# Performance work log

Measured on AMD Instinct MI355X. Metric: run time of the kernel, lower is better.

Reference implementation:

```python
import jax, jax.numpy as jnp
import numpy as np

B, T, N, F = 8, 32, 10000, 16
E = 160000
HG, HT = 64, 128
EPS = 1e-5


def setup_inputs() -> dict:
    key = jax.random.key(0)
    ks = jax.random.split(key, 12)
    s = lambda i, shape, sc=0.05: jax.random.normal(ks[i], shape, dtype=jnp.float32) * sc
    return {
        "x_seq": jax.random.normal(ks[0], (B, T, N, F), dtype=jnp.float32),
        "edge_index": jax.random.randint(ks[1], (2, E), 0, N),
        "W1l": s(2, (HG, F)), "b1": jnp.zeros((HG,), jnp.float32), "W1r": s(3, (HG, F)),
        "g1": jnp.ones((HG,), jnp.float32), "be1": jnp.zeros((HG,), jnp.float32),
        "W2l": s(4, (HG, HG)), "b2": jnp.zeros((HG,), jnp.float32), "W2r": s(5, (HG, HG)),
        "g2": jnp.ones((HG,), jnp.float32), "be2": jnp.zeros((HG,), jnp.float32),
        "W_ih": s(6, (3 * HT, HG)), "W_hh": s(7, (3 * HT, HT)),
        "b_ih": jnp.zeros((3 * HT,), jnp.float32), "b_hh": jnp.zeros((3 * HT,), jnp.float32),
        "Wh": s(8, (1, HT)), "bh": jnp.zeros((1,), jnp.float32),
    }


def _layernorm(h, g, b):
    mu = h.mean(-1, keepdims=True)
    var = ((h - mu) ** 2).mean(-1, keepdims=True)
    return (h - mu) * jax.lax.rsqrt(var + EPS) * g + b


def reference(x_seq, edge_index, W1l, b1, W1r, g1, be1, W2l, b2, W2r, g2, be2,
              W_ih, W_hh, b_ih, b_hh, Wh, bh):
    src, dst = edge_index[0], edge_index[1]
    deg = jax.ops.segment_sum(jnp.ones((E,), x_seq.dtype), dst, num_segments=N)
    inv_deg = (1.0 / jnp.maximum(deg, 1.0))[:, None]  # [N,1]

    def aggregate(x):  # x: [B,N,F] -> mean over incoming neighbors per node
        msgs = x[:, src, :]  # [B,E,F] gather
        agg = jax.vmap(lambda m: jax.ops.segment_sum(m, dst, num_segments=N))(msgs)
        return agg * inv_deg

    def sage(x, Wl, bl, Wr, g, b):
        # PyG SAGEConv(mean): lin_l(agg) + lin_r(x); then LayerNorm + ReLU (dropout=eval)
        h = aggregate(x) @ Wl.T + bl + x @ Wr.T
        return jax.nn.relu(_layernorm(h, g, b))

    def step(_, xt):  # xt: [B,N,F] -> pooled [B,HG]
        h = sage(xt, W1l, b1, W1r, g1, be1)
        h = sage(h, W2l, b2, W2r, g2, be2)
        return None, h.mean(axis=1)

    _, H = jax.lax.scan(step, None, jnp.swapaxes(x_seq, 0, 1))  # [T,B,HG]

    def gru_step(h, x):  # PyTorch GRU gate order: r, z, n
        gi = x @ W_ih.T + b_ih
        gh = h @ W_hh.T + b_hh
        ir, iz, in_ = jnp.split(gi, 3, axis=-1)
        hr, hz, hn = jnp.split(gh, 3, axis=-1)
        r = jax.nn.sigmoid(ir + hr)
        z = jax.nn.sigmoid(iz + hz)
        n = jnp.tanh(in_ + r * hn)
        return (1.0 - z) * n + z * h, None

    h0 = jnp.zeros((x_seq.shape[0], HT), x_seq.dtype)
    ht, _ = jax.lax.scan(gru_step, h0, H)
    return (ht @ Wh.T + bh).squeeze(-1)  # [B]
```

## Files before the change

kernel.cpp:

```cpp
#include <hip/hip_runtime.h>
#include <hip/hip_bf16.h>
#include <math.h>

#define B_ 8
#define T_ 32
#define N_ 10000
#define F_ 16
#define E_ 160000
#define HG_ 64
#define HT_ 128
#define BT_ (B_*T_)
#define PB_ 157
#define EPS_ 1e-5f
#define NR_ (N_+1)

typedef __attribute__((ext_vector_type(8))) short bf16x8_t;
typedef __attribute__((ext_vector_type(4))) float f32x4_t;
typedef __attribute__((ext_vector_type(2))) float f32x2_t;

__device__ inline unsigned short f2bf(float f) {
  unsigned u = __float_as_uint(f);
  u += 0x7fffu + ((u >> 16) & 1u);
  return (unsigned short)(u >> 16);
}
__device__ inline unsigned pack2bf(float a, float b) {
  __hip_bfloat162 h2 = __float22bfloat162_rn(float2{a, b});
  unsigned u;
  __builtin_memcpy(&u, &h2, 4);
  return u;
}
__device__ inline void accp(f32x2_t& a, unsigned u) {
  f32x2_t t = { __uint_as_float(u << 16), __uint_as_float(u & 0xffff0000u) };
  a += t;
}
__device__ inline void bfly2(f32x2_t& a, int m) {
  f32x2_t t = { __shfl_xor(a.x, m), __shfl_xor(a.y, m) };
  a += t;
}

__global__ void k_zero(int* p, int n) {
  int i = blockIdx.x * 256 + threadIdx.x;
  if (i < n) p[i] = 0;
}

__global__ void k_deg(const int* __restrict__ dst, int* __restrict__ deg) {
  int e = blockIdx.x * 256 + threadIdx.x;
  if (e < E_) atomicAdd(&deg[dst[e]], 1);
}

__global__ void k_scan(const int* __restrict__ deg, int* __restrict__ row_ptr,
                       float* __restrict__ inv_deg) {
  __shared__ int part[256];
  int tid = threadIdx.x;
  int base = tid * 40;
  int s = 0;
  for (int i = 0; i < 40; i++) { int idx = base + i; if (idx < N_) s += deg[idx]; }
  part[tid] = s;
  __syncthreads();
  if (tid == 0) {
    int run = 0;
    for (int i = 0; i < 256; i++) { int v = part[i]; part[i] = run; run += v; }
  }
  __syncthreads();
  int run = part[tid];
  for (int i = 0; i < 40; i++) {
    int idx = base + i;
    if (idx < N_) {
      row_ptr[idx] = run;
      int d = deg[idx];
      run += d;
      inv_deg[idx] = 1.0f / fmaxf((float)d, 1.0f);
    } else if (idx == N_) {
      row_ptr[N_] = run;
    }
  }
}

__global__ void k_fill(const int* __restrict__ src, const int* __restrict__ dst,
                       const int* __restrict__ row_ptr, int* __restrict__ cursor,
                       int* __restrict__ col) {
  int e = blockIdx.x * 256 + threadIdx.x;
  if (e < E_) {
    int d = dst[e];
    int p = atomicAdd(&cursor[d], 1);
    col[row_ptr[d] + p] = src[e];
  }
}

__global__ void k_prepw(const float* __restrict__ W2l, const float* __restrict__ W2r,
                        unsigned short* __restrict__ Wbf) {
  int idx = blockIdx.x * 256 + threadIdx.x;
  if (idx >= 4 * 4 * 64 * 8) return;
  int q  = idx & 7;
  int l  = (idx >> 3) & 63;
  int ks = (idx >> 9) & 3;
  int w  = idx >> 11;
  int j = w * 16 + (l & 15);
  int k = ks * 32 + ((l >> 4) * 8) + q;
  float v = (k < 64) ? W2l[j * 64 + k] : W2r[j * 64 + (k - 64)];
  Wbf[idx] = f2bf(v);
}

__global__ void k_prepw1(const float* __restrict__ W1l, const float* __restrict__ W1r,
                         unsigned short* __restrict__ Wb1) {
  int idx = blockIdx.x * 256 + threadIdx.x;
  if (idx >= 4 * 64 * 8) return;
  int q = idx & 7;
  int l = (idx >> 3) & 63;
  int w = idx >> 9;
  int j = w * 16 + (l & 15);
  int k = ((l >> 4) * 8) + q;
  float v = (k < 16) ? W1l[j * 16 + k] : W1r[j * 16 + (k - 16)];
  Wb1[idx] = f2bf(v);
}

__launch_bounds__(256, 8)
__global__ void k_sage1t(const float* __restrict__ x, const int* __restrict__ row_ptr,
                         const int* __restrict__ col, const float* __restrict__ inv_deg,
                         const unsigned short* __restrict__ Wb1, const float* __restrict__ b1,
                         const float* __restrict__ g1, const float* __restrict__ be1,
                         unsigned short* __restrict__ h1, const float* __restrict__ zrow,
                         int bt0, int CH, int swz) {
  __shared__ __align__(16) unsigned short ZU[64 * 136];
  __shared__ float red[2][4][64];
  unsigned short* Z1b = ZU;
  float* Zf = (float*)ZU;
  int i = blockIdx.x;
  int btl, chunk;
  if (swz) {
    int xcd = i & 7; int j = i >> 3; int per = CH >> 3;
    btl = xcd * per + j / PB_; chunk = j % PB_;
  } else {
    btl = i / PB_; chunk = i % PB_;
  }
  int bt = bt0 + btl;
  size_t xbase = (size_t)bt * (N_ * F_);
  int tid = threadIdx.x;
  int w = __builtin_amdgcn_readfirstlane(tid >> 6);
  int lane = tid & 63;
  int n0 = chunk * 64;
  int node = lane >> 4;
  int eo2 = (lane >> 2) & 3;
  int fq2 = lane & 3;
  const float4* x4b = (const float4*)(x + xbase);
  const float4* z4 = (const float4*)zrow;

  for (int p = 0; p < 4; ++p) {
    int mA = w * 16 + p * 4;
    int nA = n0 + mA;
    int s0A = 0, dA = 0, s0B = 0, dB = 0, s0C = 0, dC = 0, s0D = 0, dD = 0;
    float ivA = 0.f, ivB = 0.f, ivC = 0.f, ivD = 0.f;
    if (nA < N_)     { s0A = row_ptr[nA];   dA = row_ptr[nA+1] - s0A; ivA = inv_deg[nA]; }
    if (nA+1 < N_)   { s0B = row_ptr[nA+1]; dB = row_ptr[nA+2] - s0B; ivB = inv_deg[nA+1]; }
    if (nA+2 < N_)   { s0C = row_ptr[nA+2]; dC = row_ptr[nA+3] - s0C; ivC = inv_deg[nA+2]; }
    if (nA+3 < N_)   { s0D = row_ptr[nA+3]; dD = row_ptr[nA+4] - s0D; ivD = inv_deg[nA+3]; }
    int s0My = node < 2 ? (node ? s0B : s0A) : (node == 2 ? s0C : s0D);
    int dMy  = node < 2 ? (node ? dB  : dA)  : (node == 2 ? dC  : dD);
    float ivMy = node < 2 ? (node ? ivB : ivA) : (node == 2 ? ivC : ivD);
    int dcMy = dMy > 64 ? 64 : dMy;
    int dcA = dA > 64 ? 64 : dA, dcB = dB > 64 ? 64 : dB;
    int dcC = dC > 64 ? 64 : dC, dcD = dD > 64 ? 64 : dD;
    int mx = max(max(dcA, dcB), max(dcC, dcD));
    int rounds = (mx + 3) >> 2;
    int pos = lane & 15;
    int c0r = (pos      < dMy) ? col[s0My + pos]      : 0;
    int c1r = (pos + 16 < dMy) ? col[s0My + pos + 16] : 0;
    int c2r = (pos + 32 < dMy) ? col[s0My + pos + 32] : 0;
    int c3r = (pos + 48 < dMy) ? col[s0My + pos + 48] : 0;
    float4 a = {0.f, 0.f, 0.f, 0.f};
    int r = 0;
#define S1BODY(REG, BASE)                                             \
    {                                                                 \
      int idx = eo2 + 4 * r;                                          \
      int s = __shfl(REG, (lane & 48) | (idx - BASE));                \
      const float4* bp = (idx < dcMy) ? (x4b + (size_t)s * 4) : z4;   \
      float4 v = bp[fq2];                                             \
      a.x += v.x; a.y += v.y; a.z += v.z; a.w += v.w;                 \
    }
    for (; r < rounds && r < 4; ++r)  S1BODY(c0r, 0)
    for (; r < rounds && r < 8; ++r)  S1BODY(c1r, 16)
    for (; r < rounds && r < 12; ++r) S1BODY(c2r, 32)
    for (; r < rounds; ++r)           S1BODY(c3r, 48)
#undef S1BODY
    if (dMy > 64) {
      for (int e = s0My + 64; e < s0My + dMy; ++e) {
        if (eo2 == 0) {
          float4 v = x4b[(size_t)col[e] * 4 + fq2];
          a.x += v.x; a.y += v.y; a.z += v.z; a.w += v.w;
        }
      }
    }
    a.x += __shfl_xor(a.x, 4);  a.y += __shfl_xor(a.y, 4);
    a.z += __shfl_xor(a.z, 4);  a.w += __shfl_xor(a.w, 4);
    a.x += __shfl_xor(a.x, 8);  a.y += __shfl_xor(a.y, 8);
    a.z += __shfl_xor(a.z, 8);  a.w += __shfl_xor(a.w, 8);
    if (eo2 == 0) {
      uint2 pk;
      pk.x = pack2bf(a.x * ivMy, a.y * ivMy);
      pk.y = pack2bf(a.z * ivMy, a.w * ivMy);
      *(uint2*)&Z1b[(mA + node) * 40 + fq2 * 4] = pk;
    } else if (eo2 == 1) {
      int nS = nA + node;
      float4 sv = {0.f, 0.f, 0.f, 0.f};
      if (nS < N_) sv = x4b[(size_t)nS * 4 + fq2];
      uint2 pk;
      pk.x = pack2bf(sv.x, sv.y);
      pk.y = pack2bf(sv.z, sv.w);
      *(uint2*)&Z1b[(mA + node) * 40 + 16 + fq2 * 4] = pk;
    }
  }
  __syncthreads();

  int g = lane >> 4, c = lane & 15;
  float bj = b1[w * 16 + c];
  f32x4_t accf[4];
#pragma unroll
  for (int mt = 0; mt < 4; ++mt) accf[mt] = (f32x4_t){bj, bj, bj, bj};
  bf16x8_t bfr = ((const bf16x8_t*)Wb1)[w * 64 + lane];
#pragma unroll
  for (int mt = 0; mt < 4; ++mt) {
    const bf16x8_t* ap = (const bf16x8_t*)&Z1b[(mt * 16 + c) * 40 + g * 8];
    accf[mt] = __builtin_amdgcn_mfma_f32_16x16x32_bf16(*ap, bfr, accf[mt], 0, 0, 0);
  }
  __syncthreads();

#pragma unroll
  for (int mt = 0; mt < 4; ++mt) {
#pragma unroll
    for (int q = 0; q < 4; ++q) {
      int nodeq = mt * 16 + g * 4 + q;
      Zf[nodeq * 68 + w * 16 + c] = accf[mt][q];
    }
  }
  __syncthreads();

  int m = lane;
  const float* zr = Zf + m * 68 + w * 16;
  float4 z0 = *(const float4*)(zr + 0);
  float4 z1 = *(const float4*)(zr + 4);
  float4 z2 = *(const float4*)(zr + 8);
  float4 z3 = *(const float4*)(zr + 12);
  float acc[16];
  acc[0] = z0.x; acc[1] = z0.y; acc[2] = z0.z; acc[3] = z0.w;
  acc[4] = z1.x; acc[5] = z1.y; acc[6] = z1.z; acc[7] = z1.w;
  acc[8] = z2.x; acc[9] = z2.y; acc[10] = z2.z; acc[11] = z2.w;
  acc[12] = z3.x; acc[13] = z3.y; acc[14] = z3.z; acc[15] = z3.w;

  float s1 = 0.f, s2 = 0.f;
#pragma unroll
  for (int jj = 0; jj < 16; ++jj) { s1 += acc[jj]; s2 += acc[jj] * acc[jj]; }
  red[0][w][m] = s1;
  red[1][w][m] = s2;
  __syncthreads();
  float mu = (red[0][0][m] + red[0][1][m] + red[0][2][m] + red[0][3][m]) * (1.f / 64.f);
  float ex2 = (red[1][0][m] + red[1][1][m] + red[1][2][m] + red[1][3][m]) * (1.f / 64.f);
  float var = fmaxf(ex2 - mu * mu, 0.f);
  float rs = rsqrtf(var + EPS_);

  int nAbs = n0 + m;
  unsigned short* dst = h1 + ((size_t)btl * NR_ + nAbs) * HG_ + w * 16;
  if (nAbs < N_) {
#pragma unroll
    for (int jj = 0; jj < 16; ++jj)
      acc[jj] = fmaxf((acc[jj] - mu) * rs * g1[w * 16 + jj] + be1[w * 16 + jj], 0.f);
    uint4 pa, pb;
    pa.x = pack2bf(acc[0], acc[1]);  pa.y = pack2bf(acc[2], acc[3]);
    pa.z = pack2bf(acc[4], acc[5]);  pa.w = pack2bf(acc[6], acc[7]);
    pb.x = pack2bf(acc[8], acc[9]);  pb.y = pack2bf(acc[10], acc[11]);
    pb.z = pack2bf(acc[12], acc[13]); pb.w = pack2bf(acc[14], acc[15]);
    *(uint4*)dst = pa;
    *(uint4*)(dst + 8) = pb;
  } else if (nAbs == N_) {
    uint4 zz = {0, 0, 0, 0};
    *(uint4*)dst = zz;
    *(uint4*)(dst + 8) = zz;
  }
}

__launch_bounds__(256, 8)
__global__ void k_sage2t(const unsigned short* __restrict__ h1, const int* __restrict__ row_ptr,
                         const int* __restrict__ col, const float* __restrict__ inv_deg,
                         const unsigned short* __restrict__ Wbf, const float* __restrict__ b2,
                         const float* __restrict__ g2, const float* __restrict__ be2,
                         float* __restrict__ Hsum, int bt0, int CH, int swz) {
  __shared__ __align__(16) unsigned short Zb[64 * 136];
  __shared__ float red[2][4][64];
  float* Zf = (float*)Zb;
  int i = blockIdx.x;
  int btl, chunk;
  if (swz) {
    int xcd = i & 7; int j = i >> 3; int per = CH >> 3;
    btl = xcd * per + j / PB_; chunk = j % PB_;
  } else {
    btl = i / PB_; chunk = i % PB_;
  }
  int bt = bt0 + btl;
  int b = bt / T_, t = bt % T_;
  const char* h8c = (const char*)(h1 + (size_t)btl * (NR_ * HG_));
  int tid = threadIdx.x;
  int w = __builtin_amdgcn_readfirstlane(tid >> 6);
  int lane = tid & 63;
  int n0 = chunk * 64;
  int nsel = lane >> 5;
  int eo2 = (lane >> 3) & 3;
  int fq3 = lane & 7;
  unsigned foff = (unsigned)fq3 * 16;

  for (int p = 0; p < 8; ++p) {
    int mA = w * 16 + p * 2;
    int nA = n0 + mA, nB = nA + 1;
    int s0A = 0, dA = 0, s0B = 0, dB = 0;
    float ivA = 0.f, ivB = 0.f;
    if (nA < N_) { s0A = row_ptr[nA]; dA = row_ptr[nA + 1] - s0A; ivA = inv_deg[nA]; }
    if (nB < N_) { s0B = row_ptr[nB]; dB = row_ptr[nB + 1] - s0B; ivB = inv_deg[nB]; }
    int s0My = nsel ? s0B : s0A;
    int dMy  = nsel ? dB  : dA;
    float ivMy = nsel ? ivB : ivA;
    int dcA = dA > 64 ? 64 : dA, dcB = dB > 64 ? 64 : dB;
    int mx = max(dcA, dcB);
    int rounds = (mx + 3) >> 2;
    int pos = lane & 31;
    int c0r = (pos      < dMy) ? col[s0My + pos]      : N_;
    int c1r = (pos + 32 < dMy) ? col[s0My + pos + 32] : N_;
    f32x2_t a0 = {0.f, 0.f}, a1 = {0.f, 0.f}, a2 = {0.f, 0.f}, a3 = {0.f, 0.f};
    int r = 0;
#define S2BODY(REG, BASE)                                               \
    {                                                                   \
      int idx = eo2 + 4 * r;                                            \
      int s = __shfl(REG, (lane & 32) | (idx - BASE));                  \
      uint4 v = *(const uint4*)(h8c + (((unsigned)s << 7) + foff));     \
      accp(a0, v.x); accp(a1, v.y); accp(a2, v.z); accp(a3, v.w);       \
    }
    for (; r < rounds && r < 8; ++r) S2BODY(c0r, 0)
    for (; r < rounds; ++r)          S2BODY(c1r, 32)
#undef S2BODY
    if (dMy > 64) {
      for (int e = s0My + 64; e < s0My + dMy; ++e) {
        if (eo2 == 0) {
          uint4 v = *(const uint4*)(h8c + (((unsigned)col[e] << 7) + foff));
          accp(a0, v.x); accp(a1, v.y); accp(a2, v.z); accp(a3, v.w);
        }
      }
    }
    bfly2(a0, 8);  bfly2(a1, 8);  bfly2(a2, 8);  bfly2(a3, 8);
    bfly2(a0, 16); bfly2(a1, 16); bfly2(a2, 16); bfly2(a3, 16);
    if (eo2 == 0) {
      uint4 pk;
      pk.x = pack2bf(a0.x * ivMy, a0.y * ivMy);
      pk.y = pack2bf(a1.x * ivMy, a1.y * ivMy);
      pk.z = pack2bf(a2.x * ivMy, a2.y * ivMy);
      pk.w = pack2bf(a3.x * ivMy, a3.y * ivMy);
      *(uint4*)&Zb[(mA + nsel) * 136 + fq3 * 8] = pk;
    } else if (eo2 == 1) {
      int nS = nA + nsel;
      int nSc = nS < N_ ? nS : N_;
      uint4 sv = *(const uint4*)(h8c + (((unsigned)nSc << 7) + foff));
      *(uint4*)&Zb[(mA + nsel) * 136 + 64 + fq3 * 8] = sv;
    }
  }
  __syncthreads();

  int g = lane >> 4, c = lane & 15;
  const bf16x8_t* Wb8 = (const bf16x8_t*)Wbf;
  float bj = b2[w * 16 + c];
  f32x4_t accf[4];
#pragma unroll
  for (int mt = 0; mt < 4; ++mt) accf[mt] = (f32x4_t){bj, bj, bj, bj};
#pragma unroll
  for (int ks = 0; ks < 4; ++ks) {
    bf16x8_t bfr = Wb8[(w * 4 + ks) * 64 + lane];
#pragma unroll
    for (int mt = 0; mt < 4; ++mt) {
      const bf16x8_t* ap = (const bf16x8_t*)&Zb[(mt * 16 + c) * 136 + ks * 32 + g * 8];
      accf[mt] = __builtin_amdgcn_mfma_f32_16x16x32_bf16(*ap, bfr, accf[mt], 0, 0, 0);
    }
  }
  __syncthreads();

#pragma unroll
  for (int mt = 0; mt < 4; ++mt) {
#pragma unroll
    for (int q = 0; q < 4; ++q) {
      int nodeq = mt * 16 + g * 4 + q;
      Zf[nodeq * 68 + w * 16 + c] = accf[mt][q];
    }
  }
  __syncthreads();

  int m = lane;
  float* zr = Zf + m * 68 + w * 16;
  float4 z0 = *(const float4*)(zr + 0);
  float4 z1 = *(const float4*)(zr + 4);
  float4 z2 = *(const float4*)(zr + 8);
  float4 z3 = *(const float4*)(zr + 12);
  float acc[16];
  acc[0] = z0.x; acc[1] = z0.y; acc[2] = z0.z; acc[3] = z0.w;
  acc[4] = z1.x; acc[5] = z1.y; acc[6] = z1.z; acc[7] = z1.w;
  acc[8] = z2.x; acc[9] = z2.y; acc[10] = z2.z; acc[11] = z2.w;
  acc[12] = z3.x; acc[13] = z3.y; acc[14] = z3.z; acc[15] = z3.w;

  float s1 = 0.f, s2 = 0.f;
#pragma unroll
  for (int jj = 0; jj < 16; ++jj) { s1 += acc[jj]; s2 += acc[jj] * acc[jj]; }
  red[0][w][m] = s1;
  red[1][w][m] = s2;
  __syncthreads();
  float mu = (red[0][0][m] + red[0][1][m] + red[0][2][m] + red[0][3][m]) * (1.f / 64.f);
  float ex2 = (red[1][0][m] + red[1][1][m] + red[1][2][m] + red[1][3][m]) * (1.f / 64.f);
  float var = fmaxf(ex2 - mu * mu, 0.f);
  float rs = rsqrtf(var + EPS_);

  bool okm = (n0 + m) < N_;
#pragma unroll
  for (int jj = 0; jj < 16; ++jj) {
    float hv = fmaxf((acc[jj] - mu) * rs * g2[w * 16 + jj] + be2[w * 16 + jj], 0.f);
    acc[jj] = okm ? hv : 0.f;
  }
  float4 o0 = {acc[0], acc[1], acc[2], acc[3]};
  float4 o1 = {acc[4], acc[5], acc[6], acc[7]};
  float4 o2 = {acc[8], acc[9], acc[10], acc[11]};
  float4 o3 = {acc[12], acc[13], acc[14], acc[15]};
  *(float4*)(zr + 0) = o0;  *(float4*)(zr + 4) = o1;
  *(float4*)(zr + 8) = o2;  *(float4*)(zr + 12) = o3;
  __syncthreads();

  float cs = 0.f;
#pragma unroll
  for (int ii = 0; ii < 16; ++ii) cs += Zf[(w * 16 + ii) * 68 + lane];
  red[0][w][lane] = cs;
  __syncthreads();
  if (w == 0) {
    float tot = red[0][0][lane] + red[0][1][lane] + red[0][2][lane] + red[0][3][lane];
    atomicAdd(&Hsum[(t * B_ + b) * HG_ + lane], tot);
  }
}

__global__ void k_gi(const float* __restrict__ Hsum, const float* __restrict__ W_ih,
                     const float* __restrict__ b_ih, float* __restrict__ GI) {
  __shared__ float xv[64];
  int tb = blockIdx.x;
  int tid = threadIdx.x;
  if (tid < 64) xv[tid] = Hsum[tb * 64 + tid] * (1.0f / (float)N_);
  __syncthreads();
  float g = b_ih[tid];
  const float4* W4 = (const float4*)(W_ih + tid * 64);
  const float4* x4 = (const float4*)xv;
#pragma unroll
  for (int q = 0; q < 16; q++) {
    float4 w = W4[q], xq = x4[q];
    g = fmaf(xq.x, w.x, g); g = fmaf(xq.y, w.y, g);
    g = fmaf(xq.z, w.z, g); g = fmaf(xq.w, w.w, g);
  }
  GI[tb * 384 + tid] = g;
}

__global__ void k_gru(const float* __restrict__ GI, const float* __restrict__ W_hh,
                      const float* __restrict__ b_hh, const float* __restrict__ Wh,
                      const float* __restrict__ bh, float* __restrict__ out) {
  __shared__ float hL[128];
  __shared__ float ghL[384];
  __shared__ float red[128];
  int b = blockIdx.x, tid = threadIdx.x;
  if (tid < 128) hL[tid] = 0.f;
  float bhh = b_hh[tid];
  const float4* W4 = (const float4*)(W_hh + tid * 128);
  for (int t = 0; t < T_; ++t) {
    __syncthreads();
    float g = bhh;
    const float4* h4 = (const float4*)hL;
#pragma unroll
    for (int q = 0; q < 32; q++) {
      float4 w = W4[q], hv = h4[q];
      g = fmaf(hv.x, w.x, g); g = fmaf(hv.y, w.y, g);
      g = fmaf(hv.z, w.z, g); g = fmaf(hv.w, w.w, g);
    }
    ghL[tid] = g;
    __syncthreads();
    float hnew = 0.f;
    if (tid < 128) {
      const float* gi = GI + (t * B_ + b) * 384;
      float rr = 1.f / (1.f + expf(-(gi[tid] + ghL[tid])));
      float zz = 1.f / (1.f + expf(-(gi[128 + tid] + ghL[128 + tid])));
      float nn = tanhf(gi[256 + tid] + rr * ghL[256 + tid]);
      hnew = (1.f - zz) * nn + zz * hL[tid];
    }
    __syncthreads();
    if (tid < 128) hL[tid] = hnew;
  }
  __syncthreads();
  if (tid < 128) red[tid] = hL[tid] * Wh[tid];
  __syncthreads();
  if (tid == 0) {
    float s = bh[0];
    for (int k = 0; k < 128; k++) s += red[k];
    out[b] = s;
  }
}

extern "C" void kernel_launch(void* const* d_in, const int* in_sizes, int n_in,
                              void* d_out, int out_size, void* d_ws, size_t ws_size,
                              hipStream_t stream) {
  const float* x    = (const float*)d_in[0];
  const int*   ei   = (const int*)d_in[1];
  const float* W1l  = (const float*)d_in[2];
  const float* b1   = (const float*)d_in[3];
  const float* W1r  = (const float*)d_in[4];
  const float* g1   = (const float*)d_in[5];
  const float* be1  = (const float*)d_in[6];
  const float* W2l  = (const float*)d_in[7];
  const float* b2   = (const float*)d_in[8];
  const float* W2r  = (const float*)d_in[9];
  const float* g2   = (const float*)d_in[10];
  const float* be2  = (const float*)d_in[11];
  const float* W_ih = (const float*)d_in[12];
  const float* W_hh = (const float*)d_in[13];
  const float* b_ih = (const float*)d_in[14];
  const float* b_hh = (const float*)d_in[15];
  const float* Wh   = (const float*)d_in[16];
  const float* bh   = (const float*)d_in[17];
  float* out = (float*)d_out;

  char* ws = (char*)d_ws;
  size_t off = 0;
  auto alloc = [&](size_t bytes) { void* p = ws + off; off += (bytes + 255) & ~(size_t)255; return p; };
  int*   deg     = (int*)alloc((size_t)N_ * 4);
  int*   row_ptr = (int*)alloc((size_t)(N_ + 1) * 4);
  int*   cursor  = (int*)alloc((size_t)N_ * 4);
  int*   col     = (int*)alloc((size_t)E_ * 4);
  float* ivd     = (float*)alloc((size_t)N_ * 4);
  float* Hsum    = (float*)alloc((size_t)BT_ * HG_ * 4);
  float* GI      = (float*)alloc((size_t)BT_ * 384 * 4);
  unsigned short* Wbf = (unsigned short*)alloc((size_t)4 * 4 * 64 * 8 * 2);
  unsigned short* Wb1 = (unsigned short*)alloc((size_t)4 * 64 * 8 * 2);
  float* zrowp   = (float*)alloc(256);
  size_t fixed = off;
  unsigned short* h1 = (unsigned short*)(ws + off);

  size_t cap = (ws_size > fixed) ? (ws_size - fixed) : 0;
  int CH = (int)(cap / ((size_t)NR_ * HG_ * 2));
  if (CH > 64) CH = 64;
  if (CH >= 8) CH &= ~7;
  if (CH < 1) CH = 1;

  int zn = (int)(fixed / 4);
  k_zero<<<(zn + 255) / 256, 256, 0, stream>>>((int*)ws, zn);

  const int* srcp = ei;
  const int* dstp = ei + E_;
  k_deg<<<(E_ + 255) / 256, 256, 0, stream>>>(dstp, deg);
  k_scan<<<1, 256, 0, stream>>>(deg, row_ptr, ivd);
  k_fill<<<(E_ + 255) / 256, 256, 0, stream>>>(srcp, dstp, row_ptr, cursor, col);
  k_prepw<<<32, 256, 0, stream>>>(W2l, W2r, Wbf);
  k_prepw1<<<8, 256, 0, stream>>>(W1l, W1r, Wb1);

  for (int bt0 = 0; bt0 < BT_; bt0 += CH) {
    int c = BT_ - bt0 < CH ? BT_ - bt0 : CH;
    int swz = (c % 8 == 0) ? 1 : 0;
    k_sage1t<<<c * PB_, 256, 0, stream>>>(x, row_ptr, col, ivd, Wb1, b1, g1, be1,
                                          h1, zrowp, bt0, c, swz);
    k_sage2t<<<c * PB_, 256, 0, stream>>>(h1, row_ptr, col, ivd, Wbf, b2, g2, be2,
                                          Hsum, bt0, c, swz);
  }
  k_gi<<<BT_, 384, 0, stream>>>(Hsum, W_ih, b_ih, GI);
  k_gru<<<B_, 384, 0, stream>>>(GI, W_hh, b_hh, Wh, bh, out);
}
```

Baseline: 1.303 ms.

## Switch intermediates to fp16 with packed-half accumulation and prefetch CSR metadata

Switches the stored layer-1 activations and weights from bf16 to fp16 and uses fp16 MFMA. The layer-2 neighbor aggregation now accumulates in packed half2 instead of unpacking to fp32, which removes the conversion ALU work in the gather loop. Row pointers, degrees and column indices are loaded once per lane and spread with shuffles, the layer-2 column lists are prefetched for all passes up front, and the gather loops are unrolled by two. The cost is lower precision: summing up to 64+ neighbors in fp16 risks accuracy loss or overflow, and the prefetch arrays add register pressure.

```diff
diff --git a/kernel.cpp b/kernel.cpp
--- a/kernel.cpp
+++ b/kernel.cpp
@@ -1,5 +1,5 @@
 #include <hip/hip_runtime.h>
-#include <hip/hip_bf16.h>
+#include <hip/hip_fp16.h>
 #include <math.h>
 
 #define B_ 8
@@ -14,28 +14,29 @@
 #define EPS_ 1e-5f
 #define NR_ (N_+1)
 
-typedef __attribute__((ext_vector_type(8))) short bf16x8_t;
+typedef __attribute__((ext_vector_type(8))) _Float16 f16x8_t;
 typedef __attribute__((ext_vector_type(4))) float f32x4_t;
-typedef __attribute__((ext_vector_type(2))) float f32x2_t;
-
-__device__ inline unsigned short f2bf(float f) {
-  unsigned u = __float_as_uint(f);
-  u += 0x7fffu + ((u >> 16) & 1u);
-  return (unsigned short)(u >> 16);
-}
-__device__ inline unsigned pack2bf(float a, float b) {
-  __hip_bfloat162 h2 = __float22bfloat162_rn(float2{a, b});
-  unsigned u;
-  __builtin_memcpy(&u, &h2, 4);
-  return u;
-}
-__device__ inline void accp(f32x2_t& a, unsigned u) {
-  f32x2_t t = { __uint_as_float(u << 16), __uint_as_float(u & 0xffff0000u) };
-  a += t;
-}
-__device__ inline void bfly2(f32x2_t& a, int m) {
-  f32x2_t t = { __shfl_xor(a.x, m), __shfl_xor(a.y, m) };
-  a += t;
+
+__device__ inline unsigned short f2h(float f) {
+  return __half_as_ushort(__float2half(f));
+}
+__device__ inline unsigned pkrtz_u(float a, float b) {
+  auto h = __builtin_amdgcn_cvt_pkrtz(a, b);
+  unsigned u; __builtin_memcpy(&u, &h, 4); return u;
+}
+__device__ inline unsigned pack2h(float a, float b) {
+  __half2 h = __floats2half2_rn(a, b);
+  unsigned u; __builtin_memcpy(&u, &h, 4); return u;
+}
+__device__ inline __half2 u2h(unsigned u) {
+  __half2 h; __builtin_memcpy(&h, &u, 4); return h;
+}
+__device__ inline unsigned h2u(__half2 h) {
+  unsigned u; __builtin_memcpy(&u, &h, 4); return u;
+}
+__device__ inline void bflyh(__half2& a, int m) {
+  unsigned u = (unsigned)__shfl_xor((int)h2u(a), m);
+  a += u2h(u);
 }
 
 __global__ void k_zero(int* p, int n) {
@@ -98,7 +99,7 @@
   int j = w * 16 + (l & 15);
   int k = ks * 32 + ((l >> 4) * 8) + q;
   float v = (k < 64) ? W2l[j * 64 + k] : W2r[j * 64 + (k - 64)];
-  Wbf[idx] = f2bf(v);
+  Wbf[idx] = f2h(v);
 }
 
 __global__ void k_prepw1(const float* __restrict__ W1l, const float* __restrict__ W1r,
@@ -111,7 +112,7 @@
   int j = w * 16 + (l & 15);
   int k = ((l >> 4) * 8) + q;
   float v = (k < 16) ? W1l[j * 16 + k] : W1r[j * 16 + (k - 16)];
-  Wb1[idx] = f2bf(v);
+  Wb1[idx] = f2h(v);
 }
 
 __launch_bounds__(256, 8)
@@ -145,22 +146,19 @@
   const float4* x4b = (const float4*)(x + xbase);
   const float4* z4 = (const float4*)zrow;
 
+  int nloc = n0 + w * 16 + (lane & 15);
+  int rpA = 0, dS = 0; float ivS = 0.f;
+  if (nloc < N_) { rpA = row_ptr[nloc]; dS = row_ptr[nloc + 1] - rpA; ivS = inv_deg[nloc]; }
+
   for (int p = 0; p < 4; ++p) {
     int mA = w * 16 + p * 4;
     int nA = n0 + mA;
-    int s0A = 0, dA = 0, s0B = 0, dB = 0, s0C = 0, dC = 0, s0D = 0, dD = 0;
-    float ivA = 0.f, ivB = 0.f, ivC = 0.f, ivD = 0.f;
-    if (nA < N_)     { s0A = row_ptr[nA];   dA = row_ptr[nA+1] - s0A; ivA = inv_deg[nA]; }
-    if (nA+1 < N_)   { s0B = row_ptr[nA+1]; dB = row_ptr[nA+2] - s0B; ivB = inv_deg[nA+1]; }
-    if (nA+2 < N_)   { s0C = row_ptr[nA+2]; dC = row_ptr[nA+3] - s0C; ivC = inv_deg[nA+2]; }
-    if (nA+3 < N_)   { s0D = row_ptr[nA+3]; dD = row_ptr[nA+4] - s0D; ivD = inv_deg[nA+3]; }
-    int s0My = node < 2 ? (node ? s0B : s0A) : (node == 2 ? s0C : s0D);
-    int dMy  = node < 2 ? (node ? dB  : dA)  : (node == 2 ? dC  : dD);
-    float ivMy = node < 2 ? (node ? ivB : ivA) : (node == 2 ? ivC : ivD);
+    int s0My   = __shfl(rpA, p * 4 + node);
+    int dMy    = __shfl(dS,  p * 4 + node);
+    float ivMy = __shfl(ivS, p * 4 + node);
     int dcMy = dMy > 64 ? 64 : dMy;
-    int dcA = dA > 64 ? 64 : dA, dcB = dB > 64 ? 64 : dB;
-    int dcC = dC > 64 ? 64 : dC, dcD = dD > 64 ? 64 : dD;
-    int mx = max(max(dcA, dcB), max(dcC, dcD));
+    int tmx = max(dcMy, __shfl_xor(dcMy, 16));
+    int mx  = max(tmx, __shfl_xor(tmx, 32));
     int rounds = (mx + 3) >> 2;
     int pos = lane & 15;
     int c0r = (pos      < dMy) ? col[s0My + pos]      : 0;
@@ -168,20 +166,21 @@
     int c2r = (pos + 32 < dMy) ? col[s0My + pos + 32] : 0;
     int c3r = (pos + 48 < dMy) ? col[s0My + pos + 48] : 0;
     float4 a = {0.f, 0.f, 0.f, 0.f};
-    int r = 0;
-#define S1BODY(REG, BASE)                                             \
+#define S1B(REG, BASE, RR)                                            \
     {                                                                 \
-      int idx = eo2 + 4 * r;                                          \
-      int s = __shfl(REG, (lane & 48) | (idx - BASE));                \
+      int idx = eo2 + 4 * (RR);                                       \
+      int s = __shfl(REG, (lane & 48) | (idx - (BASE)));              \
       const float4* bp = (idx < dcMy) ? (x4b + (size_t)s * 4) : z4;   \
       float4 v = bp[fq2];                                             \
       a.x += v.x; a.y += v.y; a.z += v.z; a.w += v.w;                 \
     }
-    for (; r < rounds && r < 4; ++r)  S1BODY(c0r, 0)
-    for (; r < rounds && r < 8; ++r)  S1BODY(c1r, 16)
-    for (; r < rounds && r < 12; ++r) S1BODY(c2r, 32)
-    for (; r < rounds; ++r)           S1BODY(c3r, 48)
-#undef S1BODY
+    int rounds2 = (rounds + 1) & ~1;
+    int r = 0;
+    for (; r < rounds2 && r < 4;  r += 2) { S1B(c0r, 0, r)  S1B(c0r, 0, r + 1) }
+    for (; r < rounds2 && r < 8;  r += 2) { S1B(c1r, 16, r) S1B(c1r, 16, r + 1) }
+    for (; r < rounds2 && r < 12; r += 2) { S1B(c2r, 32, r) S1B(c2r, 32, r + 1) }
+    for (; r < rounds2; r += 2)           { S1B(c3r, 48, r) S1B(c3r, 48, r + 1) }
+#undef S1B
     if (dMy > 64) {
       for (int e = s0My + 64; e < s0My + dMy; ++e) {
         if (eo2 == 0) {
@@ -196,16 +195,16 @@
     a.z += __shfl_xor(a.z, 8);  a.w += __shfl_xor(a.w, 8);
     if (eo2 == 0) {
       uint2 pk;
-      pk.x = pack2bf(a.x * ivMy, a.y * ivMy);
-      pk.y = pack2bf(a.z * ivMy, a.w * ivMy);
+      pk.x = pkrtz_u(a.x * ivMy, a.y * ivMy);
+      pk.y = pkrtz_u(a.z * ivMy, a.w * ivMy);
       *(uint2*)&Z1b[(mA + node) * 40 + fq2 * 4] = pk;
     } else if (eo2 == 1) {
       int nS = nA + node;
       float4 sv = {0.f, 0.f, 0.f, 0.f};
       if (nS < N_) sv = x4b[(size_t)nS * 4 + fq2];
       uint2 pk;
-      pk.x = pack2bf(sv.x, sv.y);
-      pk.y = pack2bf(sv.z, sv.w);
+      pk.x = pkrtz_u(sv.x, sv.y);
+      pk.y = pkrtz_u(sv.z, sv.w);
       *(uint2*)&Z1b[(mA + node) * 40 + 16 + fq2 * 4] = pk;
     }
   }
@@ -216,11 +215,11 @@
   f32x4_t accf[4];
 #pragma unroll
   for (int mt = 0; mt < 4; ++mt) accf[mt] = (f32x4_t){bj, bj, bj, bj};
-  bf16x8_t bfr = ((const bf16x8_t*)Wb1)[w * 64 + lane];
+  f16x8_t bfr = ((const f16x8_t*)Wb1)[w * 64 + lane];
 #pragma unroll
   for (int mt = 0; mt < 4; ++mt) {
-    const bf16x8_t* ap = (const bf16x8_t*)&Z1b[(mt * 16 + c) * 40 + g * 8];
-    accf[mt] = __builtin_amdgcn_mfma_f32_16x16x32_bf16(*ap, bfr, accf[mt], 0, 0, 0);
+    const f16x8_t* ap = (const f16x8_t*)&Z1b[(mt * 16 + c) * 40 + g * 8];
+    accf[mt] = __builtin_amdgcn_mfma_f32_16x16x32_f16(*ap, bfr, accf[mt], 0, 0, 0);
   }
   __syncthreads();
 
@@ -264,10 +263,10 @@
     for (int jj = 0; jj < 16; ++jj)
       acc[jj] = fmaxf((acc[jj] - mu) * rs * g1[w * 16 + jj] + be1[w * 16 + jj], 0.f);
     uint4 pa, pb;
-    pa.x = pack2bf(acc[0], acc[1]);  pa.y = pack2bf(acc[2], acc[3]);
-    pa.z = pack2bf(acc[4], acc[5]);  pa.w = pack2bf(acc[6], acc[7]);
-    pb.x = pack2bf(acc[8], acc[9]);  pb.y = pack2bf(acc[10], acc[11]);
-    pb.z = pack2bf(acc[12], acc[13]); pb.w = pack2bf(acc[14], acc[15]);
+    pa.x = pack2h(acc[0], acc[1]);  pa.y = pack2h(acc[2], acc[3]);
+    pa.z = pack2h(acc[4], acc[5]);  pa.w = pack2h(acc[6], acc[7]);
+    pb.x = pack2h(acc[8], acc[9]);  pb.y = pack2h(acc[10], acc[11]);
+    pb.z = pack2h(acc[12], acc[13]); pb.w = pack2h(acc[14], acc[15]);
     *(uint4*)dst = pa;
     *(uint4*)(dst + 8) = pb;
   } else if (nAbs == N_) {
@@ -305,53 +304,61 @@
   int eo2 = (lane >> 3) & 3;
   int fq3 = lane & 7;
   unsigned foff = (unsigned)fq3 * 16;
-
+  int pos = lane & 31;
+
+  int nloc = n0 + w * 16 + (lane & 15);
+  int rpA = 0, dS = 0; float ivS = 0.f;
+  if (nloc < N_) { rpA = row_ptr[nloc]; dS = row_ptr[nloc + 1] - rpA; ivS = inv_deg[nloc]; }
+
+  int cp0[8], cp1[8];
+#pragma unroll
+  for (int p = 0; p < 8; ++p) {
+    int s0 = __shfl(rpA, p * 2 + nsel);
+    int d  = __shfl(dS,  p * 2 + nsel);
+    cp0[p] = (pos      < d) ? col[s0 + pos]      : N_;
+    cp1[p] = (pos + 32 < d) ? col[s0 + pos + 32] : N_;
+  }
+
+#pragma unroll
   for (int p = 0; p < 8; ++p) {
     int mA = w * 16 + p * 2;
-    int nA = n0 + mA, nB = nA + 1;
-    int s0A = 0, dA = 0, s0B = 0, dB = 0;
-    float ivA = 0.f, ivB = 0.f;
-    if (nA < N_) { s0A = row_ptr[nA]; dA = row_ptr[nA + 1] - s0A; ivA = inv_deg[nA]; }
-    if (nB < N_) { s0B = row_ptr[nB]; dB = row_ptr[nB + 1] - s0B; ivB = inv_deg[nB]; }
-    int s0My = nsel ? s0B : s0A;
-    int dMy  = nsel ? dB  : dA;
-    float ivMy = nsel ? ivB : ivA;
-    int dcA = dA > 64 ? 64 : dA, dcB = dB > 64 ? 64 : dB;
-    int mx = max(dcA, dcB);
+    int s0My   = __shfl(rpA, p * 2 + nsel);
+    int dMy    = __shfl(dS,  p * 2 + nsel);
+    float ivMy = __shfl(ivS, p * 2 + nsel);
+    int dcMy = dMy > 64 ? 64 : dMy;
+    int mx = max(dcMy, __shfl_xor(dcMy, 32));
     int rounds = (mx + 3) >> 2;
-    int pos = lane & 31;
-    int c0r = (pos      < dMy) ? col[s0My + pos]      : N_;
-    int c1r = (pos + 32 < dMy) ? col[s0My + pos + 32] : N_;
-    f32x2_t a0 = {0.f, 0.f}, a1 = {0.f, 0.f}, a2 = {0.f, 0.f}, a3 = {0.f, 0.f};
+    __half2 a0 = __float2half2_rn(0.f), a1 = a0, a2 = a0, a3 = a0;
+#define S2B(PREG, BASE, RR)                                             \
+    {                                                                   \
+      int idx = eo2 + 4 * (RR);                                         \
+      int s = __shfl(PREG, (lane & 32) | (idx - (BASE)));               \
+      uint4 v = *(const uint4*)(h8c + (((unsigned)s << 7) + foff));     \
+      a0 += u2h(v.x); a1 += u2h(v.y); a2 += u2h(v.z); a3 += u2h(v.w);   \
+    }
+    int rounds2 = (rounds + 1) & ~1;
     int r = 0;
-#define S2BODY(REG, BASE)                                               \
-    {                                                                   \
-      int idx = eo2 + 4 * r;                                            \
-      int s = __shfl(REG, (lane & 32) | (idx - BASE));                  \
-      uint4 v = *(const uint4*)(h8c + (((unsigned)s << 7) + foff));     \
-      accp(a0, v.x); accp(a1, v.y); accp(a2, v.z); accp(a3, v.w);       \
-    }
-    for (; r < rounds && r < 8; ++r) S2BODY(c0r, 0)
-    for (; r < rounds; ++r)          S2BODY(c1r, 32)
-#undef S2BODY
+    for (; r < rounds2 && r < 8; r += 2) { S2B(cp0[p], 0, r)  S2B(cp0[p], 0, r + 1) }
+    for (; r < rounds2; r += 2)          { S2B(cp1[p], 32, r) S2B(cp1[p], 32, r + 1) }
+#undef S2B
     if (dMy > 64) {
       for (int e = s0My + 64; e < s0My + dMy; ++e) {
         if (eo2 == 0) {
           uint4 v = *(const uint4*)(h8c + (((unsigned)col[e] << 7) + foff));
-          accp(a0, v.x); accp(a1, v.y); accp(a2, v.z); accp(a3, v.w);
+          a0 += u2h(v.x); a1 += u2h(v.y); a2 += u2h(v.z); a3 += u2h(v.w);
         }
       }
     }
-    bfly2(a0, 8);  bfly2(a1, 8);  bfly2(a2, 8);  bfly2(a3, 8);
-    bfly2(a0, 16); bfly2(a1, 16); bfly2(a2, 16); bfly2(a3, 16);
+    bflyh(a0, 8);  bflyh(a1, 8);  bflyh(a2, 8);  bflyh(a3, 8);
+    bflyh(a0, 16); bflyh(a1, 16); bflyh(a2, 16); bflyh(a3, 16);
     if (eo2 == 0) {
+      __half2 ivh = __float2half2_rn(ivMy);
       uint4 pk;
-      pk.x = pack2bf(a0.x * ivMy, a0.y * ivMy);
-      pk.y = pack2bf(a1.x * ivMy, a1.y * ivMy);
-      pk.z = pack2bf(a2.x * ivMy, a2.y * ivMy);
-      pk.w = pack2bf(a3.x * ivMy, a3.y * ivMy);
+      pk.x = h2u(a0 * ivh); pk.y = h2u(a1 * ivh);
+      pk.z = h2u(a2 * ivh); pk.w = h2u(a3 * ivh);
       *(uint4*)&Zb[(mA + nsel) * 136 + fq3 * 8] = pk;
     } else if (eo2 == 1) {
+      int nA = n0 + mA;
       int nS = nA + nsel;
       int nSc = nS < N_ ? nS : N_;
       uint4 sv = *(const uint4*)(h8c + (((unsigned)nSc << 7) + foff));
@@ -361,18 +368,18 @@
   __syncthreads();
 
   int g = lane >> 4, c = lane & 15;
-  const bf16x8_t* Wb8 = (const bf16x8_t*)Wbf;
+  const f16x8_t* Wb8 = (const f16x8_t*)Wbf;
   float bj = b2[w * 16 + c];
   f32x4_t accf[4];
 #pragma unroll
   for (int mt = 0; mt < 4; ++mt) accf[mt] = (f32x4_t){bj, bj, bj, bj};
 #pragma unroll
   for (int ks = 0; ks < 4; ++ks) {
-    bf16x8_t bfr = Wb8[(w * 4 + ks) * 64 + lane];
+    f16x8_t bfr = Wb8[(w * 4 + ks) * 64 + lane];
 #pragma unroll
     for (int mt = 0; mt < 4; ++mt) {
-      const bf16x8_t* ap = (const bf16x8_t*)&Zb[(mt * 16 + c) * 136 + ks * 32 + g * 8];
-      accf[mt] = __builtin_amdgcn_mfma_f32_16x16x32_bf16(*ap, bfr, accf[mt], 0, 0, 0);
+      const f16x8_t* ap = (const f16x8_t*)&Zb[(mt * 16 + c) * 136 + ks * 32 + g * 8];
+      accf[mt] = __builtin_amdgcn_mfma_f32_16x16x32_f16(*ap, bfr, accf[mt], 0, 0, 0);
     }
   }
   __syncthreads();
```

After: 1.164 ms (median of 2 runs). -10.7%, faster.
